# Optimization experiments

Hardware: AMD Instinct MI355X
Metric: run time of the kernel (lower is better)

Reference implementation:

```python
import jax, jax.numpy as jnp
import numpy as np

F = 128      # n_features
NRBF = 6     # radial basis size
NSH = 7      # spherical basis size (SbfLayer(N_shbf, N_shbf, c))
NBIL = 8     # bilinear dim
CUT = 5.0    # cutoff c
NA = 4096    # atoms
NE = 65536   # edges
NT = 262144  # triplets
NB = 64      # molecules in batch
NZ = 95      # atom types


def _swish(x):
    return x * jax.nn.sigmoid(x)


def setup_inputs():
    key = jax.random.key(0)
    ks = list(jax.random.split(key, 32))
    def nrm(k, shape, s):
        return jax.random.normal(k, shape, dtype=jnp.float32) * s
    inp = {}
    inp['Z'] = jax.random.randint(ks[0], (NA,), 0, NZ)
    inp['R'] = jax.random.normal(ks[1], (NA, 3), dtype=jnp.float32)
    inp['batch_seg'] = jnp.sort(jax.random.randint(ks[2], (NA,), 0, NB))
    inp['idnb_i'] = jax.random.randint(ks[3], (NE,), 0, NA)
    inp['idnb_j'] = jax.random.randint(ks[4], (NE,), 0, NA)
    inp['id_expand_kj'] = jax.random.randint(ks[5], (NT,), 0, NE)
    inp['id_reduce_ji'] = jax.random.randint(ks[6], (NT,), 0, NE)
    inp['id3dnb_i'] = jax.random.randint(ks[7], (NT,), 0, NA)
    inp['id3dnb_j'] = jax.random.randint(ks[8], (NT,), 0, NA)
    inp['id3dnb_k'] = jax.random.randint(ks[9], (NT,), 0, NA)
    # learned parameters
    inp['emb'] = nrm(ks[10], (NZ, F), 0.1)
    inp['W_emb'] = nrm(ks[11], (2 * F + NRBF, F), 0.05)
    inp['b_emb'] = jnp.zeros((F,), jnp.float32)
    inp['out_Wrbf'] = nrm(ks[12], (8, NRBF, F), 0.05)
    inp['out_W1'] = nrm(ks[13], (8, F, F), 0.05)
    inp['out_b1'] = jnp.zeros((8, F), jnp.float32)
    inp['out_W2'] = nrm(ks[14], (8, F, 1), 0.05)
    inp['int_Wrbf'] = nrm(ks[15], (7, NRBF, F), 0.05)
    inp['int_Wsbf'] = nrm(ks[16], (7, NSH * NSH, NBIL), 0.05)
    inp['int_Wkj'] = nrm(ks[17], (7, F, F), 0.05)
    inp['int_bkj'] = jnp.zeros((7, F), jnp.float32)
    inp['int_Wji'] = nrm(ks[18], (7, F, F), 0.05)
    inp['int_bji'] = jnp.zeros((7, F), jnp.float32)
    inp['int_Wbil'] = nrm(ks[19], (7, F, NBIL, F), 0.02)
    inp['int_Wfin'] = nrm(ks[20], (7, F, F), 0.05)
    inp['int_bfin'] = jnp.zeros((7, F), jnp.float32)
    return inp


def _forward(Z, R, batch_seg, idnb_i, idnb_j, id_expand_kj, id_reduce_ji,
             id3dnb_i, id3dnb_j, id3dnb_k,
             emb, W_emb, b_emb,
             out_Wrbf, out_W1, out_b1, out_W2,
             int_Wrbf, int_Wsbf, int_Wkj, int_bkj, int_Wji, int_bji,
             int_Wbil, int_Wfin, int_bfin):
    n_atoms = Z.shape[0]
    n_edges = idnb_i.shape[0]
    # interatomic distances Dij [E]
    diff = R[idnb_i] - R[idnb_j]
    Dij = jnp.sqrt(jax.nn.relu(jnp.sum(diff * diff, -1)))
    dsafe = jnp.maximum(Dij, 1e-6)
    # radial Bessel basis [E, NRBF]
    n = jnp.arange(1, NRBF + 1, dtype=R.dtype)
    rbf = jnp.sqrt(2.0 / CUT) * jnp.sin(n * jnp.pi * dsafe[:, None] / CUT) / dsafe[:, None]
    # triplet angles via cross/atan2 [T]
    R1 = R[id3dnb_j] - R[id3dnb_i]
    R2 = R[id3dnb_k] - R[id3dnb_i]
    x = jnp.sum(R1 * R2, -1)
    y = jnp.linalg.norm(jnp.cross(R1, R2), axis=-1)
    ang = jnp.arctan2(y, x)
    # spherical basis: radial(d_kj) x angular(cos(l*theta)) -> [T, NSH*NSH]
    d_kj = jnp.maximum(Dij[id_expand_kj], 1e-6)
    nr = jnp.arange(1, NSH + 1, dtype=R.dtype)
    radial = jnp.sin(nr * jnp.pi * d_kj[:, None] / CUT) / d_kj[:, None]       # [T, NSH]
    ls = jnp.arange(NSH, dtype=R.dtype)
    angular = jnp.cos(ls[None, :] * ang[:, None])                              # [T, NSH]
    sbf = (angular[:, :, None] * radial[:, None, :]).reshape(ang.shape[0], NSH * NSH)
    # embedding: edge messages m [E, F]
    h = emb[Z]
    m = _swish(jnp.concatenate([h[idnb_i], h[idnb_j], rbf], -1) @ W_emb + b_emb)

    def out_layer(m, k):
        t = m * (rbf @ out_Wrbf[k])                                            # [E, F]
        ta = jax.ops.segment_sum(t, idnb_i, num_segments=n_atoms)             # [A, F]
        ta = _swish(ta @ out_W1[k] + out_b1[k])
        return ta @ out_W2[k]                                                  # [A, 1]

    P = out_layer(m, 0)
    for i in range(7):
        x_ji = _swish(m @ int_Wji[i] + int_bji[i])
        x_kj = _swish(m @ int_Wkj[i] + int_bkj[i]) * (rbf @ int_Wrbf[i])       # [E, F]
        x_kj = x_kj[id_expand_kj]                                              # [T, F]
        sb = sbf @ int_Wsbf[i]                                                 # [T, NBIL]
        x_kj = jnp.einsum('wl,wj,jli->wi', sb, x_kj, int_Wbil[i])             # [T, F]
        x_kj = jax.ops.segment_sum(x_kj, id_reduce_ji, num_segments=n_edges)  # [E, F]
        m = m + _swish((x_ji + x_kj) @ int_Wfin[i] + int_bfin[i])
        P = P + out_layer(m, i + 1)
    return jax.ops.segment_sum(P, batch_seg, num_segments=NB)                 # [NB, 1]


def reference(Z, R, batch_seg, idnb_i, idnb_j, id_expand_kj, id_reduce_ji,
              id3dnb_i, id3dnb_j, id3dnb_k,
              emb, W_emb, b_emb,
              out_Wrbf, out_W1, out_b1, out_W2,
              int_Wrbf, int_Wsbf, int_Wkj, int_bkj, int_Wji, int_bji,
              int_Wbil, int_Wfin, int_bfin):
    return _forward(Z, R, batch_seg, idnb_i, idnb_j, id_expand_kj, id_reduce_ji,
                    id3dnb_i, id3dnb_j, id3dnb_k,
                    emb, W_emb, b_emb,
                    out_Wrbf, out_W1, out_b1, out_W2,
                    int_Wrbf, int_Wsbf, int_Wkj, int_bkj, int_Wji, int_bji,
                    int_Wbil, int_Wfin, int_bfin)
```

## Files before the change

### kernel.cpp

```cpp
#include <hip/hip_runtime.h>

typedef __attribute__((ext_vector_type(8))) short shortx8;
typedef __attribute__((ext_vector_type(4))) float floatx4;
typedef __attribute__((ext_vector_type(4))) unsigned uintx4;

constexpr int NAc = 4096;
constexpr int NEc = 65536;
constexpr int NTc = 262144;
constexpr float PI_F = 3.14159265358979323846f;
constexpr float SQ25 = 0.63245553203367587f;

__device__ __forceinline__ float bf2f(unsigned short h){ return __uint_as_float(((unsigned)h)<<16); }
__device__ __forceinline__ unsigned short f2bf(float f){
  unsigned u = __float_as_uint(f);
  u += 0x7fffu + ((u>>16)&1u);
  return (unsigned short)(u>>16);
}
__device__ __forceinline__ float swishf(float x){ return x/(1.f+__expf(-x)); }

__device__ __forceinline__ floatx4 mfma16x16x32bf(shortx8 a, shortx8 b, floatx4 c){
  floatx4 d;
  asm("v_mfma_f32_16x16x32_bf16 %0, %1, %2, %3" : "=v"(d) : "v"(a), "v"(b), "v"(c));
  return d;
}

__global__ __launch_bounds__(256)
void egeom_k(const float* __restrict__ R, const int* __restrict__ ei,
             const int* __restrict__ ej, float* __restrict__ Dij, float* __restrict__ rbf){
  int e = blockIdx.x*256 + threadIdx.x;
  int i = ei[e], j = ej[e];
  float dx = R[i*3+0]-R[j*3+0];
  float dy = R[i*3+1]-R[j*3+1];
  float dz = R[i*3+2]-R[j*3+2];
  float d2 = dx*dx+dy*dy+dz*dz;
  float D = sqrtf(fmaxf(d2, 0.f));
  Dij[e] = D;
  float d = fmaxf(D, 1e-6f);
  float s = PI_F*d*0.2f;
  float sn, cs; sincosf(s, &sn, &cs);
  float invd = SQ25/d;
  float sprev = 0.f, scur = sn;
  #pragma unroll
  for (int q=0;q<6;q++){
    rbf[e*6+q] = scur*invd;
    float nx = 2.f*cs*scur - sprev; sprev = scur; scur = nx;
  }
}

__global__ __launch_bounds__(256)
void tgeom_k(const float* __restrict__ R, const int* __restrict__ t3i,
             const int* __restrict__ t3j, const int* __restrict__ t3k,
             const int* __restrict__ texp, const int* __restrict__ tperm,
             const float* __restrict__ Dij, float* __restrict__ angp,
             int* __restrict__ tmeta){
  int p = blockIdx.x*256 + threadIdx.x;
  int w = tperm[p];
  int ia = t3i[w], ja = t3j[w], ka = t3k[w];
  int e  = texp[w];
  tmeta[p] = e;
  float xi = R[ia*3+0], yi = R[ia*3+1], zi = R[ia*3+2];
  float r1x = R[ja*3+0]-xi, r1y = R[ja*3+1]-yi, r1z = R[ja*3+2]-zi;
  float r2x = R[ka*3+0]-xi, r2y = R[ka*3+1]-yi, r2z = R[ka*3+2]-zi;
  float dt = r1x*r2x + r1y*r2y + r1z*r2z;
  float cx = r1y*r2z - r1z*r2y;
  float cy = r1z*r2x - r1x*r2z;
  float cz = r1x*r2y - r1y*r2x;
  float yv = sqrtf(cx*cx + cy*cy + cz*cz);
  float h = sqrtf(dt*dt + yv*yv);
  float c1 = (h > 0.f) ? dt/h : 1.f;
  float f[16];
  f[0] = 1.f; f[1] = c1;
  float cprev = 1.f, ccur = c1;
  #pragma unroll
  for (int l=2;l<7;l++){
    float nx = 2.f*c1*ccur - cprev; cprev = ccur; ccur = nx;
    f[l] = nx;
  }
  float d = fmaxf(Dij[e], 1e-6f);
  float s = PI_F*d*0.2f;
  float sn, cs; sincosf(s, &sn, &cs);
  float invd = 1.f/d;
  float sprev = 0.f, scur = sn;
  #pragma unroll
  for (int q=0;q<7;q++){
    f[7+q] = scur*invd;
    float nx = 2.f*cs*scur - sprev; sprev = scur; scur = nx;
  }
  f[14] = 0.f; f[15] = 0.f;
  float4* op = (float4*)(angp + (size_t)p*16);
  op[0] = (float4){f[0],f[1],f[2],f[3]};
  op[1] = (float4){f[4],f[5],f[6],f[7]};
  op[2] = (float4){f[8],f[9],f[10],f[11]};
  op[3] = (float4){f[12],f[13],f[14],f[15]};
}

__global__ __launch_bounds__(256)
void prep_transpose(const float* __restrict__ Wemb, const float* __restrict__ Wji,
                    const float* __restrict__ Wkj, const float* __restrict__ Wfin,
                    unsigned short* __restrict__ dW12, unsigned short* __restrict__ dWjk,
                    unsigned short* __restrict__ dWfin){
  int y = blockIdx.y;
  int x = blockIdx.x*256 + threadIdx.x;
  if (y == 0){
    if (x < 32768){
      int n = x >> 8, k = x & 255;
      dW12[x] = f2bf(Wemb[k*128 + n]);
    }
  } else {
    if (x < 16384){
      int n = x >> 7, k = x & 127;
      const float* s; unsigned short* d;
      if (y <= 7)      { s = Wji  + (y-1)*16384;  d = dWjk  + (y-1)*32768; }
      else if (y <= 14){ s = Wkj  + (y-8)*16384;  d = dWjk  + (y-8)*32768 + 16384; }
      else             { s = Wfin + (y-15)*16384; d = dWfin + (y-15)*16384; }
      d[x] = f2bf(s[k*128 + n]);
    }
  }
}

__global__ __launch_bounds__(256)
void prep_wbil(const float* __restrict__ Wbil, unsigned short* __restrict__ dst){
  int x = blockIdx.x*256 + threadIdx.x;
  if (x < 7*131072){
    int i = x >> 17; int rem = x & 131071;
    int o = rem >> 10; int k = rem & 1023;
    dst[x] = f2bf(Wbil[(size_t)i*131072 + (size_t)k*128 + o]);
  }
}

__global__ __launch_bounds__(256)
void prep_emb(const float* __restrict__ emb, unsigned short* __restrict__ d){
  int x = blockIdx.x*256 + threadIdx.x;
  if (x < 95*128) d[x] = f2bf(emb[x]);
}

__global__ __launch_bounds__(256)
void hist_k(const int* __restrict__ ids, int n, int* __restrict__ hist){
  int stride = gridDim.x*blockDim.x;
  for (int x = blockIdx.x*blockDim.x + threadIdx.x; x < n; x += stride)
    atomicAdd(&hist[ids[x]], 1);
}

__global__ __launch_bounds__(256)
void scan1_k(const int* __restrict__ hist, int* __restrict__ offs, int* __restrict__ bsum){
  __shared__ int buf[256];
  int t = threadIdx.x;
  int x = blockIdx.x*256 + t;
  int v = hist[x];
  buf[t] = v; __syncthreads();
  #pragma unroll
  for (int d=1; d<256; d<<=1){
    int u = (t>=d) ? buf[t-d] : 0;
    __syncthreads(); buf[t] += u; __syncthreads();
  }
  offs[x] = buf[t] - v;
  if (t == 255) bsum[blockIdx.x] = buf[255];
}

__global__ __launch_bounds__(256)
void scan2_k(int* __restrict__ bsum, int nb){
  __shared__ int buf[256];
  int t = threadIdx.x;
  int v = (t < nb) ? bsum[t] : 0;
  buf[t] = v; __syncthreads();
  #pragma unroll
  for (int d=1; d<256; d<<=1){
    int u = (t>=d) ? buf[t-d] : 0;
    __syncthreads(); buf[t] += u; __syncthreads();
  }
  if (t < nb) bsum[t] = buf[t] - v;
}

__global__ __launch_bounds__(256)
void scan3_k(const int* __restrict__ hist, int* __restrict__ offs,
             const int* __restrict__ bsum, int nbins){
  int x = blockIdx.x*256 + threadIdx.x;
  int o = offs[x] + bsum[blockIdx.x];
  offs[x] = o;
  if (x == nbins-1) offs[nbins] = o + hist[x];
}

__global__ __launch_bounds__(256)
void scatter_k(const int* __restrict__ ids, int n, const int* __restrict__ offs,
               int* __restrict__ cursor, int* __restrict__ perm){
  int stride = gridDim.x*blockDim.x;
  for (int x = blockIdx.x*blockDim.x + threadIdx.x; x < n; x += stride){
    int b = ids[x];
    int pos = offs[b] + atomicAdd(&cursor[b], 1);
    perm[pos] = x;
  }
}

__global__ __launch_bounds__(256)
void sb_k(const float* __restrict__ angp, const float* __restrict__ Wsbf,
          float* __restrict__ sb){
  __shared__ float Ws[392];
  for (int x = threadIdx.x; x < 392; x += 256) Ws[x] = Wsbf[x];
  __syncthreads();
  int p = blockIdx.x*256 + threadIdx.x;
  const float4* ap = (const float4*)(angp + (size_t)p*16);
  float4 a0 = ap[0], a1 = ap[1], a2 = ap[2], a3 = ap[3];
  float ca[7] = {a0.x,a0.y,a0.z,a0.w,a1.x,a1.y,a1.z};
  float rd[7] = {a1.w,a2.x,a2.y,a2.z,a2.w,a3.x,a3.y};
  float o[8] = {0,0,0,0,0,0,0,0};
  #pragma unroll
  for (int a=0;a<7;a++){
    #pragma unroll
    for (int r=0;r<7;r++){
      float pr = ca[a]*rd[r];
      const float* wp = &Ws[(a*7+r)*8];
      #pragma unroll
      for (int l=0;l<8;l++) o[l] += pr*wp[l];
    }
  }
  float4* op = (float4*)(sb + (size_t)p*8);
  op[0] = (float4){o[0],o[1],o[2],o[3]};
  op[1] = (float4){o[4],o[5],o[6],o[7]};
}

__global__ __launch_bounds__(256)
void gbuild_k(int c0, const int* __restrict__ toffs, const int* __restrict__ tmeta,
              const float* __restrict__ sb, const unsigned short* __restrict__ xkj,
              unsigned short* __restrict__ G){
  int lane = threadIdx.x & 63;
  int wv = __builtin_amdgcn_readfirstlane(threadIdx.x >> 6);
  int r = c0 + blockIdx.x*4 + wv;
  float acc0[8] = {}, acc1[8] = {};
  int s = toffs[r], e_ = toffs[r+1];
  for (int t = s; t < e_; t += 4){
    int tl = e_ - 1;
    int t1 = (t+1 < e_) ? t+1 : tl;
    int t2 = (t+2 < e_) ? t+2 : tl;
    int t3 = (t+3 < e_) ? t+3 : tl;
    float w1 = (t+1 < e_) ? 1.f : 0.f;
    float w2 = (t+2 < e_) ? 1.f : 0.f;
    float w3 = (t+3 < e_) ? 1.f : 0.f;
    int e0 = tmeta[t], e1 = tmeta[t1], e2 = tmeta[t2], e3 = tmeta[t3];
    unsigned xv0 = *(const unsigned*)&xkj[(size_t)e0*128 + lane*2];
    unsigned xv1 = *(const unsigned*)&xkj[(size_t)e1*128 + lane*2];
    unsigned xv2 = *(const unsigned*)&xkj[(size_t)e2*128 + lane*2];
    unsigned xv3 = *(const unsigned*)&xkj[(size_t)e3*128 + lane*2];
    float4 sa0 = *(const float4*)&sb[(size_t)t *8];
    float4 sc0 = *(const float4*)&sb[(size_t)t *8 + 4];
    float4 sa1 = *(const float4*)&sb[(size_t)t1*8];
    float4 sc1 = *(const float4*)&sb[(size_t)t1*8 + 4];
    float4 sa2 = *(const float4*)&sb[(size_t)t2*8];
    float4 sc2 = *(const float4*)&sb[(size_t)t2*8 + 4];
    float4 sa3 = *(const float4*)&sb[(size_t)t3*8];
    float4 sc3 = *(const float4*)&sb[(size_t)t3*8 + 4];
    float x00 = bf2f((unsigned short)(xv0 & 0xffffu));
    float x01 = bf2f((unsigned short)(xv0 >> 16));
    float x10 = bf2f((unsigned short)(xv1 & 0xffffu)) * w1;
    float x11 = bf2f((unsigned short)(xv1 >> 16)) * w1;
    float x20 = bf2f((unsigned short)(xv2 & 0xffffu)) * w2;
    float x21 = bf2f((unsigned short)(xv2 >> 16)) * w2;
    float x30 = bf2f((unsigned short)(xv3 & 0xffffu)) * w3;
    float x31 = bf2f((unsigned short)(xv3 >> 16)) * w3;
    acc0[0] += sa0.x*x00 + sa1.x*x10 + sa2.x*x20 + sa3.x*x30;
    acc1[0] += sa0.x*x01 + sa1.x*x11 + sa2.x*x21 + sa3.x*x31;
    acc0[1] += sa0.y*x00 + sa1.y*x10 + sa2.y*x20 + sa3.y*x30;
    acc1[1] += sa0.y*x01 + sa1.y*x11 + sa2.y*x21 + sa3.y*x31;
    acc0[2] += sa0.z*x00 + sa1.z*x10 + sa2.z*x20 + sa3.z*x30;
    acc1[2] += sa0.z*x01 + sa1.z*x11 + sa2.z*x21 + sa3.z*x31;
    acc0[3] += sa0.w*x00 + sa1.w*x10 + sa2.w*x20 + sa3.w*x30;
    acc1[3] += sa0.w*x01 + sa1.w*x11 + sa2.w*x21 + sa3.w*x31;
    acc0[4] += sc0.x*x00 + sc1.x*x10 + sc2.x*x20 + sc3.x*x30;
    acc1[4] += sc0.x*x01 + sc1.x*x11 + sc2.x*x21 + sc3.x*x31;
    acc0[5] += sc0.y*x00 + sc1.y*x10 + sc2.y*x20 + sc3.y*x30;
    acc1[5] += sc0.y*x01 + sc1.y*x11 + sc2.y*x21 + sc3.y*x31;
    acc0[6] += sc0.z*x00 + sc1.z*x10 + sc2.z*x20 + sc3.z*x30;
    acc1[6] += sc0.z*x01 + sc1.z*x11 + sc2.z*x21 + sc3.z*x31;
    acc0[7] += sc0.w*x00 + sc1.w*x10 + sc2.w*x20 + sc3.w*x30;
    acc1[7] += sc0.w*x01 + sc1.w*x11 + sc2.w*x21 + sc3.w*x31;
  }
  size_t base = (size_t)(r - c0)*1024 + (size_t)lane*16;
  uintx4 v0, v1;
  #pragma unroll
  for (int d=0; d<4; d++){
    v0[d] = (unsigned)f2bf(acc0[2*d]) | ((unsigned)f2bf(acc0[2*d+1]) << 16);
    v1[d] = (unsigned)f2bf(acc1[2*d]) | ((unsigned)f2bf(acc1[2*d+1]) << 16);
  }
  *(uintx4*)&G[base]     = v0;
  *(uintx4*)&G[base + 8] = v1;
}

template<int MODE, int EPI>
__global__ __launch_bounds__(256)
void gemm_k(const unsigned short* __restrict__ A, const unsigned short* __restrict__ Bt,
            int K, int rowoff, int arow0,
            const int* __restrict__ gi, const int* __restrict__ gj, const int* __restrict__ Zr,
            const float* __restrict__ rbfp, const float* __restrict__ W6,
            const float* __restrict__ bias, const float* __restrict__ bias2,
            const float* minp, const unsigned short* __restrict__ xjip,
            float* outF, unsigned short* outB, unsigned short* outB2){
  __shared__ __align__(16) unsigned short As[64*72];
  __shared__ __align__(16) unsigned short Bs[128*72];
  const int tid = threadIdx.x;
  const int lane = tid & 63;
  const int wid = tid >> 6;
  const int wr = wid >> 1, wc = wid & 1;
  const int rowbase = rowoff + blockIdx.x*64;
  const int brow0 = (EPI==5) ? (int)blockIdx.y*128 : 0;
  floatx4 acc[2][4];
  #pragma unroll
  for (int i=0;i<2;i++)
    #pragma unroll
    for (int j=0;j<4;j++) acc[i][j] = (floatx4){0.f,0.f,0.f,0.f};

  for (int k0 = 0; k0 < K; k0 += 64){
    shortx8 ra[2], rb[4];
    #pragma unroll
    for (int q=0;q<2;q++){
      int c = q*256 + tid;
      int row = c >> 3;
      int ko = (c & 7) << 3;
      const unsigned short* asrc;
      if (MODE == 0){
        asrc = A + (size_t)(rowbase - arow0 + row)*K + k0 + ko;
      } else {
        int grow = rowbase + row;
        int kg = k0 + ko;
        int atom = (kg < 128) ? gi[grow] : gj[grow];
        asrc = A + (size_t)Zr[atom]*128 + (kg & 127);
      }
      ra[q] = *(const shortx8*)asrc;
    }
    #pragma unroll
    for (int q=0;q<4;q++){
      int c = q*256 + tid;
      int row = c >> 3;
      int ko = (c & 7) << 3;
      rb[q] = *(const shortx8*)(Bt + (size_t)(brow0 + row)*K + k0 + ko);
    }
    __syncthreads();
    #pragma unroll
    for (int q=0;q<2;q++){
      int c = q*256 + tid;
      *(shortx8*)&As[(c>>3)*72 + ((c&7)<<3)] = ra[q];
    }
    #pragma unroll
    for (int q=0;q<4;q++){
      int c = q*256 + tid;
      *(shortx8*)&Bs[(c>>3)*72 + ((c&7)<<3)] = rb[q];
    }
    __syncthreads();
    #pragma unroll
    for (int kk=0; kk<2; kk++){
      shortx8 af[2], bfr[4];
      #pragma unroll
      for (int mi=0;mi<2;mi++)
        af[mi] = *(const shortx8*)&As[(wr*32 + mi*16 + (lane&15))*72 + kk*32 + ((lane>>4)<<3)];
      #pragma unroll
      for (int ni=0;ni<4;ni++)
        bfr[ni] = *(const shortx8*)&Bs[(wc*64 + ni*16 + (lane&15))*72 + kk*32 + ((lane>>4)<<3)];
      #pragma unroll
      for (int mi=0;mi<2;mi++)
        #pragma unroll
        for (int ni=0;ni<4;ni++)
          acc[mi][ni] = mfma16x16x32bf(af[mi], bfr[ni], acc[mi][ni]);
    }
  }
  asm volatile("s_nop 7\ns_nop 7\ns_nop 7");

  #pragma unroll
  for (int mi=0;mi<2;mi++){
    #pragma unroll
    for (int j=0;j<4;j++){
      int row = wr*32 + mi*16 + ((lane>>4)<<2) + j;
      int grow = rowbase + row;
      float rb6[6];
      bool needr = (EPI==0) || ((EPI==5) && blockIdx.y==1);
      if (needr){
        #pragma unroll
        for (int q=0;q<6;q++) rb6[q] = rbfp[grow*6+q];
      }
      #pragma unroll
      for (int ni=0;ni<4;ni++){
        int col = wc*64 + ni*16 + (lane&15);
        float v = acc[mi][ni][j];
        size_t oidx = (size_t)grow*128 + col;
        if (EPI==0){
          float e = bias[col];
          #pragma unroll
          for (int q=0;q<6;q++) e += rb6[q]*W6[q*128+col];
          v = swishf(v + e);
          outF[oidx] = v;
          outB[oidx] = f2bf(v);
        } else if (EPI==3){
          v += bf2f(xjip[oidx]);
          outB[oidx] = f2bf(v);
        } else if (EPI==4){
          float nm = minp[oidx] + swishf(v + bias[col]);
          outF[oidx] = nm;
          outB[oidx] = f2bf(nm);
        } else {
          if (blockIdx.y == 0){
            v = swishf(v + bias[col]);
            outB[oidx] = f2bf(v);
          } else {
            float rp = 0.f;
            #pragma unroll
            for (int q=0;q<6;q++) rp += rb6[q]*W6[q*128+col];
            v = swishf(v + bias2[col]) * rp;
            outB2[oidx] = f2bf(v);
          }
        }
      }
    }
  }
}

__global__ __launch_bounds__(256)
void out_layer_k(const int* __restrict__ eperm, const int* __restrict__ eoffs,
                 const unsigned short* __restrict__ mbf, const float* __restrict__ rbf,
                 const float* __restrict__ Wrbf, const float* __restrict__ W1,
                 const float* __restrict__ b1, const float* __restrict__ W2,
                 const int* __restrict__ bseg, float* __restrict__ out){
  __shared__ float ta_lds[4][128];
  int lane = threadIdx.x & 63;
  int wv = __builtin_amdgcn_readfirstlane(threadIdx.x >> 6);
  int a = blockIdx.x*4 + wv;
  int f0 = lane*2;
  float wr0[6], wr1[6];
  #pragma unroll
  for (int q=0;q<6;q++){ wr0[q] = Wrbf[q*128+f0]; wr1[q] = Wrbf[q*128+f0+1]; }
  float ta0 = 0.f, ta1 = 0.f;
  int s = eoffs[a], e_ = eoffs[a+1];
  for (int t = s; t < e_; t++){
    int e = eperm[t];
    unsigned mv = *(const unsigned*)&mbf[(size_t)e*128 + f0];
    float r0 = rbf[e*6+0], r1 = rbf[e*6+1], r2 = rbf[e*6+2];
    float r3 = rbf[e*6+3], r4 = rbf[e*6+4], r5 = rbf[e*6+5];
    float rp0 = r0*wr0[0]+r1*wr0[1]+r2*wr0[2]+r3*wr0[3]+r4*wr0[4]+r5*wr0[5];
    float rp1 = r0*wr1[0]+r1*wr1[1]+r2*wr1[2]+r3*wr1[3]+r4*wr1[4]+r5*wr1[5];
    ta0 += bf2f((unsigned short)(mv & 0xffffu))*rp0;
    ta1 += bf2f((unsigned short)(mv >> 16))*rp1;
  }
  ta_lds[wv][f0]   = ta0;
  ta_lds[wv][f0+1] = ta1;
  float p = 0.f;
  #pragma unroll
  for (int h=0; h<2; h++){
    int n = lane + h*64;
    float o = b1[n];
    for (int f=0; f<128; f++) o += ta_lds[wv][f]*W1[f*128+n];
    p += swishf(o)*W2[n];
  }
  #pragma unroll
  for (int off=32; off; off>>=1) p += __shfl_down(p, off);
  if (lane == 0) atomicAdd(&out[bseg[a]], p);
}

extern "C" void kernel_launch(void* const* d_in, const int* in_sizes, int n_in,
                              void* d_out, int out_size, void* d_ws, size_t ws_size,
                              hipStream_t stream){
  const int*   Z    = (const int*)d_in[0];
  const float* R    = (const float*)d_in[1];
  const int*   bseg = (const int*)d_in[2];
  const int*   ei   = (const int*)d_in[3];
  const int*   ej   = (const int*)d_in[4];
  const int*   texp = (const int*)d_in[5];
  const int*   tred = (const int*)d_in[6];
  const int*   t3i  = (const int*)d_in[7];
  const int*   t3j  = (const int*)d_in[8];
  const int*   t3k  = (const int*)d_in[9];
  const float* emb  = (const float*)d_in[10];
  const float* Wemb = (const float*)d_in[11];
  const float* bemb = (const float*)d_in[12];
  const float* oWr  = (const float*)d_in[13];
  const float* oW1  = (const float*)d_in[14];
  const float* ob1  = (const float*)d_in[15];
  const float* oW2  = (const float*)d_in[16];
  const float* iWr  = (const float*)d_in[17];
  const float* iWs  = (const float*)d_in[18];
  const float* iWkj = (const float*)d_in[19];
  const float* ibkj = (const float*)d_in[20];
  const float* iWji = (const float*)d_in[21];
  const float* ibji = (const float*)d_in[22];
  const float* iWb  = (const float*)d_in[23];
  const float* iWf  = (const float*)d_in[24];
  const float* ibf  = (const float*)d_in[25];
  float* out = (float*)d_out;

  char* p = (char*)d_ws;
  auto alloc = [&](size_t bytes)->char*{ char* r = p; p += (bytes + 255) & ~(size_t)255; return r; };
  float* Dij    = (float*)alloc((size_t)NEc*4);
  float* rbf    = (float*)alloc((size_t)NEc*6*4);
  float* angp   = (float*)alloc((size_t)NTc*16*4);
  float* sball  = (float*)alloc((size_t)NTc*8*4);
  float* m      = (float*)alloc((size_t)NEc*128*4);
  unsigned short* mbf  = (unsigned short*)alloc((size_t)NEc*128*2);
  unsigned short* xji  = (unsigned short*)alloc((size_t)NEc*128*2);
  unsigned short* xkj  = (unsigned short*)alloc((size_t)NEc*128*2);
  unsigned short* afin = (unsigned short*)alloc((size_t)NEc*128*2);
  int* thist = (int*)alloc((size_t)NEc*4);
  int* toffs = (int*)alloc((size_t)(NEc+1)*4);
  int* tperm = (int*)alloc((size_t)NTc*4);
  int* tmeta = (int*)alloc((size_t)NTc*4);
  int* ehist = (int*)alloc((size_t)NAc*4);
  int* eoffs = (int*)alloc((size_t)(NAc+1)*4);
  int* eperm = (int*)alloc((size_t)NEc*4);
  int* bsum  = (int*)alloc((size_t)257*4);
  unsigned short* embbf = (unsigned short*)alloc((size_t)95*128*2);
  unsigned short* W12et = (unsigned short*)alloc((size_t)128*256*2);
  unsigned short* Wjkt  = (unsigned short*)alloc((size_t)7*32768*2);
  unsigned short* Wfint = (unsigned short*)alloc((size_t)7*16384*2);
  unsigned short* Wbilt = (unsigned short*)alloc((size_t)7*131072*2);
  size_t fixed = (size_t)(p - (char*)d_ws);

  int nch = 1;
  while (nch < 8 && fixed + ((size_t)NEc/nch)*1024*2 > ws_size) nch <<= 1;
  int ECH = NEc / nch;
  unsigned short* Gbuf = (unsigned short*)alloc((size_t)ECH*1024*2);

  hipMemsetAsync(d_out, 0, 64*sizeof(float), stream);
  hipMemsetAsync(thist, 0, (size_t)NEc*4, stream);
  hipMemsetAsync(ehist, 0, (size_t)NAc*4, stream);

  prep_transpose<<<dim3(128,22),256,0,stream>>>(Wemb, iWji, iWkj, iWf, W12et, Wjkt, Wfint);
  prep_wbil<<<3584,256,0,stream>>>(iWb, Wbilt);
  prep_emb<<<48,256,0,stream>>>(emb, embbf);
  egeom_k<<<NEc/256,256,0,stream>>>(R, ei, ej, Dij, rbf);

  hist_k<<<512,256,0,stream>>>(tred, NTc, thist);
  scan1_k<<<NEc/256,256,0,stream>>>(thist, toffs, bsum);
  scan2_k<<<1,256,0,stream>>>(bsum, NEc/256);
  scan3_k<<<NEc/256,256,0,stream>>>(thist, toffs, bsum, NEc);
  hipMemsetAsync(thist, 0, (size_t)NEc*4, stream);
  scatter_k<<<512,256,0,stream>>>(tred, NTc, toffs, thist, tperm);
  hist_k<<<256,256,0,stream>>>(ei, NEc, ehist);
  scan1_k<<<NAc/256,256,0,stream>>>(ehist, eoffs, bsum);
  scan2_k<<<1,256,0,stream>>>(bsum, NAc/256);
  scan3_k<<<NAc/256,256,0,stream>>>(ehist, eoffs, bsum, NAc);
  hipMemsetAsync(ehist, 0, (size_t)NAc*4, stream);
  scatter_k<<<256,256,0,stream>>>(ei, NEc, eoffs, ehist, eperm);

  tgeom_k<<<NTc/256,256,0,stream>>>(R, t3i, t3j, t3k, texp, tperm, Dij, angp, tmeta);

  gemm_k<1,0><<<NEc/64,256,0,stream>>>(embbf, W12et, 256, 0, 0, ei, ej, Z,
      rbf, Wemb + 256*128, bemb, nullptr, nullptr, nullptr, m, mbf, nullptr);
  out_layer_k<<<NAc/4,256,0,stream>>>(eperm, eoffs, mbf, rbf,
                                      oWr, oW1, ob1, oW2, bseg, out);

  for (int i=0;i<7;i++){
    sb_k<<<NTc/256,256,0,stream>>>(angp, iWs + i*392, sball);
    gemm_k<0,5><<<dim3(NEc/64,2),256,0,stream>>>(mbf, Wjkt + i*32768, 128, 0, 0,
        nullptr, nullptr, nullptr, rbf, iWr + i*768, ibji + i*128, ibkj + i*128,
        nullptr, nullptr, nullptr, xji, xkj);
    for (int c=0;c<nch;c++){
      int c0 = c*ECH;
      gbuild_k<<<ECH/4,256,0,stream>>>(c0, toffs, tmeta, sball, xkj, Gbuf);
      gemm_k<0,3><<<ECH/64,256,0,stream>>>(Gbuf, Wbilt + (size_t)i*131072, 1024, c0, c0,
          nullptr, nullptr, nullptr, nullptr, nullptr, nullptr, nullptr, nullptr,
          xji, nullptr, afin, nullptr);
    }
    gemm_k<0,4><<<NEc/64,256,0,stream>>>(afin, Wfint + i*16384, 128, 0, 0,
        nullptr, nullptr, nullptr, nullptr, nullptr, ibf + i*128, nullptr,
        m, nullptr, m, mbf, nullptr);
    out_layer_k<<<NAc/4,256,0,stream>>>(eperm, eoffs, mbf, rbf,
        oWr + (i+1)*768, oW1 + (i+1)*16384, ob1 + (i+1)*128, oW2 + (i+1)*128, bseg, out);
  }
  (void)in_sizes; (void)n_in; (void)out_size;
}
```

Before: 1.450 ms.

## Fuse rbf projection into GEMM epilogue and simplify output-layer gather

The embedding and update GEMM epilogues now also compute m * (rbf @ Wrbf) for the next output layer and write it as a bf16 buffer. The output-layer kernel then only gathers and sums that buffer, four edges per iteration, with no per-edge rbf loads or 6-term dot products. The chunk count for the bilinear G buffer now starts at 2, which halves the buffer size at the cost of more launches. The change adds an extra bf16 write per edge-feature in each GEMM and a new workspace buffer.

```diff
diff --git a/kernel.cpp b/kernel.cpp
--- a/kernel.cpp
+++ b/kernel.cpp
@@ -290,6 +290,7 @@
             int K, int rowoff, int arow0,
             const int* __restrict__ gi, const int* __restrict__ gj, const int* __restrict__ Zr,
             const float* __restrict__ rbfp, const float* __restrict__ W6,
+            const float* __restrict__ W6b,
             const float* __restrict__ bias, const float* __restrict__ bias2,
             const float* minp, const unsigned short* __restrict__ xjip,
             float* outF, unsigned short* outB, unsigned short* outB2){
@@ -369,7 +370,7 @@
       int row = wr*32 + mi*16 + ((lane>>4)<<2) + j;
       int grow = rowbase + row;
       float rb6[6];
-      bool needr = (EPI==0) || ((EPI==5) && blockIdx.y==1);
+      bool needr = (EPI==0) || (EPI==4) || ((EPI==5) && blockIdx.y==1);
       if (needr){
         #pragma unroll
         for (int q=0;q<6;q++) rb6[q] = rbfp[grow*6+q];
@@ -386,6 +387,10 @@
           v = swishf(v + e);
           outF[oidx] = v;
           outB[oidx] = f2bf(v);
+          float rp = 0.f;
+          #pragma unroll
+          for (int q=0;q<6;q++) rp += rb6[q]*W6b[q*128+col];
+          outB2[oidx] = f2bf(v*rp);
         } else if (EPI==3){
           v += bf2f(xjip[oidx]);
           outB[oidx] = f2bf(v);
@@ -393,6 +398,10 @@
           float nm = minp[oidx] + swishf(v + bias[col]);
           outF[oidx] = nm;
           outB[oidx] = f2bf(nm);
+          float rp = 0.f;
+          #pragma unroll
+          for (int q=0;q<6;q++) rp += rb6[q]*W6b[q*128+col];
+          outB2[oidx] = f2bf(nm*rp);
         } else {
           if (blockIdx.y == 0){
             v = swishf(v + bias[col]);
@@ -412,29 +421,38 @@
 
 __global__ __launch_bounds__(256)
 void out_layer_k(const int* __restrict__ eperm, const int* __restrict__ eoffs,
-                 const unsigned short* __restrict__ mbf, const float* __restrict__ rbf,
-                 const float* __restrict__ Wrbf, const float* __restrict__ W1,
-                 const float* __restrict__ b1, const float* __restrict__ W2,
+                 const unsigned short* __restrict__ tbuf,
+                 const float* __restrict__ W1, const float* __restrict__ b1,
+                 const float* __restrict__ W2,
                  const int* __restrict__ bseg, float* __restrict__ out){
   __shared__ float ta_lds[4][128];
   int lane = threadIdx.x & 63;
   int wv = __builtin_amdgcn_readfirstlane(threadIdx.x >> 6);
   int a = blockIdx.x*4 + wv;
   int f0 = lane*2;
-  float wr0[6], wr1[6];
-  #pragma unroll
-  for (int q=0;q<6;q++){ wr0[q] = Wrbf[q*128+f0]; wr1[q] = Wrbf[q*128+f0+1]; }
   float ta0 = 0.f, ta1 = 0.f;
   int s = eoffs[a], e_ = eoffs[a+1];
-  for (int t = s; t < e_; t++){
-    int e = eperm[t];
-    unsigned mv = *(const unsigned*)&mbf[(size_t)e*128 + f0];
-    float r0 = rbf[e*6+0], r1 = rbf[e*6+1], r2 = rbf[e*6+2];
-    float r3 = rbf[e*6+3], r4 = rbf[e*6+4], r5 = rbf[e*6+5];
-    float rp0 = r0*wr0[0]+r1*wr0[1]+r2*wr0[2]+r3*wr0[3]+r4*wr0[4]+r5*wr0[5];
-    float rp1 = r0*wr1[0]+r1*wr1[1]+r2*wr1[2]+r3*wr1[3]+r4*wr1[4]+r5*wr1[5];
-    ta0 += bf2f((unsigned short)(mv & 0xffffu))*rp0;
-    ta1 += bf2f((unsigned short)(mv >> 16))*rp1;
+  for (int t = s; t < e_; t += 4){
+    int tl = e_ - 1;
+    int t1 = (t+1 < e_) ? t+1 : tl;
+    int t2 = (t+2 < e_) ? t+2 : tl;
+    int t3 = (t+3 < e_) ? t+3 : tl;
+    float w1 = (t+1 < e_) ? 1.f : 0.f;
+    float w2 = (t+2 < e_) ? 1.f : 0.f;
+    float w3 = (t+3 < e_) ? 1.f : 0.f;
+    int e0 = eperm[t], e1 = eperm[t1], e2 = eperm[t2], e3 = eperm[t3];
+    unsigned v0 = *(const unsigned*)&tbuf[(size_t)e0*128 + f0];
+    unsigned v1 = *(const unsigned*)&tbuf[(size_t)e1*128 + f0];
+    unsigned v2 = *(const unsigned*)&tbuf[(size_t)e2*128 + f0];
+    unsigned v3 = *(const unsigned*)&tbuf[(size_t)e3*128 + f0];
+    ta0 += bf2f((unsigned short)(v0 & 0xffffu))
+         + w1*bf2f((unsigned short)(v1 & 0xffffu))
+         + w2*bf2f((unsigned short)(v2 & 0xffffu))
+         + w3*bf2f((unsigned short)(v3 & 0xffffu));
+    ta1 += bf2f((unsigned short)(v0 >> 16))
+         + w1*bf2f((unsigned short)(v1 >> 16))
+         + w2*bf2f((unsigned short)(v2 >> 16))
+         + w3*bf2f((unsigned short)(v3 >> 16));
   }
   ta_lds[wv][f0]   = ta0;
   ta_lds[wv][f0+1] = ta1;
@@ -490,6 +508,7 @@
   float* sball  = (float*)alloc((size_t)NTc*8*4);
   float* m      = (float*)alloc((size_t)NEc*128*4);
   unsigned short* mbf  = (unsigned short*)alloc((size_t)NEc*128*2);
+  unsigned short* tbuf = (unsigned short*)alloc((size_t)NEc*128*2);
   unsigned short* xji  = (unsigned short*)alloc((size_t)NEc*128*2);
   unsigned short* xkj  = (unsigned short*)alloc((size_t)NEc*128*2);
   unsigned short* afin = (unsigned short*)alloc((size_t)NEc*128*2);
@@ -508,8 +527,9 @@
   unsigned short* Wbilt = (unsigned short*)alloc((size_t)7*131072*2);
   size_t fixed = (size_t)(p - (char*)d_ws);
 
-  int nch = 1;
+  int nch = 2;
   while (nch < 8 && fixed + ((size_t)NEc/nch)*1024*2 > ws_size) nch <<= 1;
+  if (fixed + ((size_t)NEc/nch)*1024*2 > ws_size) nch = 8;
   int ECH = NEc / nch;
   unsigned short* Gbuf = (unsigned short*)alloc((size_t)ECH*1024*2);
 
@@ -538,27 +558,26 @@
   tgeom_k<<<NTc/256,256,0,stream>>>(R, t3i, t3j, t3k, texp, tperm, Dij, angp, tmeta);
 
   gemm_k<1,0><<<NEc/64,256,0,stream>>>(embbf, W12et, 256, 0, 0, ei, ej, Z,
-      rbf, Wemb + 256*128, bemb, nullptr, nullptr, nullptr, m, mbf, nullptr);
-  out_layer_k<<<NAc/4,256,0,stream>>>(eperm, eoffs, mbf, rbf,
-                                      oWr, oW1, ob1, oW2, bseg, out);
+      rbf, Wemb + 256*128, oWr, bemb, nullptr, nullptr, nullptr, m, mbf, tbuf);
+  out_layer_k<<<NAc/4,256,0,stream>>>(eperm, eoffs, tbuf, oW1, ob1, oW2, bseg, out);
 
   for (int i=0;i<7;i++){
     sb_k<<<NTc/256,256,0,stream>>>(angp, iWs + i*392, sball);
     gemm_k<0,5><<<dim3(NEc/64,2),256,0,stream>>>(mbf, Wjkt + i*32768, 128, 0, 0,
-        nullptr, nullptr, nullptr, rbf, iWr + i*768, ibji + i*128, ibkj + i*128,
+        nullptr, nullptr, nullptr, rbf, iWr + i*768, nullptr, ibji + i*128, ibkj + i*128,
         nullptr, nullptr, nullptr, xji, xkj);
     for (int c=0;c<nch;c++){
       int c0 = c*ECH;
       gbuild_k<<<ECH/4,256,0,stream>>>(c0, toffs, tmeta, sball, xkj, Gbuf);
       gemm_k<0,3><<<ECH/64,256,0,stream>>>(Gbuf, Wbilt + (size_t)i*131072, 1024, c0, c0,
           nullptr, nullptr, nullptr, nullptr, nullptr, nullptr, nullptr, nullptr,
-          xji, nullptr, afin, nullptr);
+          nullptr, xji, nullptr, afin, nullptr);
     }
     gemm_k<0,4><<<NEc/64,256,0,stream>>>(afin, Wfint + i*16384, 128, 0, 0,
-        nullptr, nullptr, nullptr, nullptr, nullptr, ibf + i*128, nullptr,
-        m, nullptr, m, mbf, nullptr);
-    out_layer_k<<<NAc/4,256,0,stream>>>(eperm, eoffs, mbf, rbf,
-        oWr + (i+1)*768, oW1 + (i+1)*16384, ob1 + (i+1)*128, oW2 + (i+1)*128, bseg, out);
+        nullptr, nullptr, nullptr, rbf, nullptr, oWr + (i+1)*768, ibf + i*128, nullptr,
+        m, nullptr, m, mbf, tbuf);
+    out_layer_k<<<NAc/4,256,0,stream>>>(eperm, eoffs, tbuf,
+        oW1 + (i+1)*16384, ob1 + (i+1)*128, oW2 + (i+1)*128, bseg, out);
   }
   (void)in_sizes; (void)n_in; (void)out_size;
 }
```

New measurement: 1.666 ms. 1.15x slower.
